# Optimization experiments

Measured on AMD Instinct MI355X. Metric: run time of the kernel, lower is better.

The kernel has to match this reference:

```python
import jax, jax.numpy as jnp
import numpy as np
import math

# Config (matches init_kwargs): ProphetNet-style ngram self-attention
T, B, E, H, NGRAM, NB, MAXD = 512, 4, 1024, 16, 2, 32, 128
HD = E // H
TGT = (1 + NGRAM) * T
NEG = -1e9


def _buckets(rel):
    # faithful numpy version of _relative_positions_bucket (bidirectional=False)
    n = np.maximum(-rel, 0)
    max_exact = NB // 2
    is_small = n < max_exact
    large = max_exact + np.log(np.maximum(n, 1) / max_exact) / math.log(MAXD / max_exact) * (NB - max_exact)
    large = np.minimum(large, NB - 1).astype(np.int32)
    return np.where(is_small, n.astype(np.int32), large)


def setup_inputs() -> dict:
    key = jax.random.key(0)
    ks = jax.random.split(key, 4)
    s = 0.02
    # position ids 1..T (ProphetNet positions start at 1); precompute bucket tables
    pos = np.arange(1, T + 1, dtype=np.int64)[None, :].repeat(B, axis=0)          # [B,T]
    main_rel = pos[:, None, :] - pos[:, :, None]                                  # [B,T,T]
    pred_keys = np.concatenate([pos - 1, pos], axis=-1)                           # [B,2T]
    pred_rel = pred_keys[:, None, :] - pos[:, :, None]                            # [B,T,2T]
    return {
        "query": jax.random.normal(ks[0], (TGT, B, E), jnp.float32),
        "in_proj_weight": jax.random.normal(ks[1], (3 * E, E), jnp.float32) * s,
        "in_proj_bias": jnp.zeros((3 * E,), jnp.float32),
        "rel_w": jax.random.normal(ks[2], (NB * H, E), jnp.float32) * s,
        "rel_b": jnp.zeros((NB * H,), jnp.float32),
        "out_w": jax.random.normal(ks[3], (E, E), jnp.float32) * s,
        "out_b": jnp.zeros((E,), jnp.float32),
        "main_buckets": jnp.asarray(_buckets(main_rel), jnp.int32),
        "predict_buckets": jnp.asarray(_buckets(pred_rel), jnp.int32),
    }


def reference(query, in_proj_weight, in_proj_bias, rel_w, rel_b, out_w, out_b,
              main_buckets, predict_buckets):
    scaling = HD ** -0.5
    qkv = query @ in_proj_weight.T + in_proj_bias                  # [TGT,B,3E]
    q, k, v = jnp.split(qkv, 3, axis=-1)
    q = q * scaling

    def heads(x):  # [TGT,B,E] -> [B*H, TGT, HD]
        return x.reshape(TGT, B * H, HD).transpose(1, 0, 2)

    q, k, v = heads(q), heads(k), heads(v)
    q_main, k_main, v_main = q[:, :T], k[:, :T], v[:, :T]

    def ngram_split(x):  # [B*H, NGRAM*T, HD] -> [N, B*H, T, HD]
        return x[:, T:].reshape(B * H, NGRAM, T, HD).transpose(1, 0, 2, 3)

    q_pred, k_pred, v_pred = ngram_split(q), ngram_split(k), ngram_split(v)
    h_main = query[:T]                                             # [T,B,E]
    h_pred = query[T:].reshape(NGRAM, T, B, E)

    # ---------- main stream ----------
    aw_main = jnp.einsum('bth,bsh->bts', q_main, k_main)           # [B*H,T,T]
    vals = h_main.transpose(1, 0, 2) @ rel_w.T + rel_b             # [B,T,NB*H]
    vals = vals.reshape(B, T, NB, H).transpose(0, 3, 1, 2)         # [B,H,T,NB]
    idx = jnp.broadcast_to(main_buckets[:, None], (B, H, T, T))
    rel_main = jnp.take_along_axis(vals, idx, axis=-1).reshape(B * H, T, T)
    causal = jnp.triu(jnp.full((T, T), NEG, jnp.float32), 1)       # self_attn_mask
    aw_main = jax.nn.softmax(aw_main + rel_main + causal[None], axis=-1)
    attn_main = jnp.einsum('bts,bsh->bth', aw_main, v_main)        # [B*H,T,HD]
    attn_main = attn_main.transpose(1, 0, 2).reshape(1, T, B, E)
    attn_main = attn_main @ out_w.T + out_b

    # ---------- ngram predict streams ----------
    k_ng = jnp.concatenate([jnp.broadcast_to(k_main[None], (NGRAM, B * H, T, HD)), k_pred], axis=2)
    v_ng = jnp.concatenate([jnp.broadcast_to(v_main[None], (NGRAM, B * H, T, HD)), v_pred], axis=2)
    aw_ng = jnp.einsum('nbtc,nbsc->nbts', q_pred, k_ng)            # [N,B*H,T,2T]
    valsn = h_pred.transpose(0, 2, 1, 3) @ rel_w.T + rel_b         # [N,B,T,NB*H]
    valsn = valsn.reshape(NGRAM, B, T, NB, H).transpose(0, 1, 4, 2, 3)  # [N,B,H,T,NB]
    idxn = jnp.broadcast_to(predict_buckets[None, :, None], (NGRAM, B, H, T, 2 * T))
    rel_ng = jnp.take_along_axis(valsn, idxn, axis=-1).reshape(NGRAM, B * H, T, 2 * T)
    # ngram_mask: main part causal, predict part only the matching position
    ng_mask = jnp.concatenate([causal, NEG * (1.0 - jnp.eye(T, dtype=jnp.float32))], axis=1)  # [T,2T]
    aw_ng = jax.nn.softmax(aw_ng + rel_ng + ng_mask[None, None], axis=-1)
    attn_ng = jnp.einsum('nbts,nbsc->nbtc', aw_ng, v_ng)           # [N,B*H,T,HD]
    attn_ng = attn_ng.transpose(0, 2, 1, 3).reshape(NGRAM, T, B, E)
    attn_ng = attn_ng @ out_w.T + out_b

    return jnp.concatenate([attn_main, attn_ng], axis=0).reshape(TGT, B, E)
```

## Files before the change

kernel.cpp:

```cpp
#include <hip/hip_runtime.h>
#include <hip/hip_bf16.h>
#include <math.h>

constexpr int T_ = 512;
constexpr int B_ = 4;
constexpr int E_ = 1024;
constexpr int H_ = 16;
constexpr int NGRAM_ = 2;
constexpr int TGT_ = (1 + NGRAM_) * T_;
constexpr int ROWS_ = TGT_ * B_;

typedef __bf16 bf16_t;
typedef __bf16 bf16x8 __attribute__((ext_vector_type(8)));
typedef __bf16 bf16x4 __attribute__((ext_vector_type(4)));
typedef float f32x4 __attribute__((ext_vector_type(4)));

#define GLL(gaddr, laddr)                                                     \
  __builtin_amdgcn_global_load_lds(                                           \
      (const __attribute__((address_space(1))) void*)(gaddr),                 \
      (__attribute__((address_space(3))) void*)(laddr), 16, 0, 0)

__global__ __launch_bounds__(256) void prep(
    const float* __restrict__ query, const float* __restrict__ ipw,
    const float* __restrict__ relw, const float* __restrict__ outw,
    bf16_t* __restrict__ qb, bf16_t* __restrict__ ipwb,
    bf16_t* __restrict__ relwb, bf16_t* __restrict__ outwb,
    const int* __restrict__ mbuck, const int* __restrict__ pbuck,
    unsigned char* __restrict__ lutM, unsigned char* __restrict__ lutP) {
  const int i = blockIdx.x * 256 + threadIdx.x;
  if (i < 512) {
    lutM[i] = (unsigned char)mbuck[(size_t)i * T_];
    lutP[i] = (unsigned char)pbuck[(size_t)i * (2 * T_)];
  }
  constexpr int N1 = ROWS_ * E_ / 4;
  constexpr int N2 = 3 * E_ * E_ / 4;
  constexpr int N3 = 512 * E_ / 4;
  constexpr int N4 = E_ * E_ / 4;
  const float4* src;
  bf16_t* dst;
  int j = i;
  if (i < N1) { src = (const float4*)query; dst = qb; }
  else if (i < N1 + N2) { src = (const float4*)ipw; dst = ipwb; j = i - N1; }
  else if (i < N1 + N2 + N3) { src = (const float4*)relw; dst = relwb; j = i - N1 - N2; }
  else if (i < N1 + N2 + N3 + N4) { src = (const float4*)outw; dst = outwb; j = i - N1 - N2 - N3; }
  else return;
  const float4 v = src[j];
  bf16x4 o;
  o[0] = (bf16_t)v.x; o[1] = (bf16_t)v.y;
  o[2] = (bf16_t)v.z; o[3] = (bf16_t)v.w;
  ((bf16x4*)dst)[j] = o;
}

__global__ __launch_bounds__(256) void transpose_v(
    const bf16_t* __restrict__ qkvb, bf16_t* __restrict__ vT) {
  __shared__ bf16_t tile[64][72];
  const int tb = blockIdx.x;
  const int bh = blockIdx.y;
  const int b = bh >> 4, h = bh & 15;
  const int tid = threadIdx.x;
  const int tau0 = tb * 64;
#pragma unroll
  for (int u = 0; u < 2; ++u) {
    const int c = u * 256 + tid;
    const int r = c >> 3, kc = c & 7;
    *(uint4*)&tile[r][kc * 8] = *(const uint4*)
        &qkvb[((size_t)(tau0 + r) * B_ + b) * 3072 + 2048 + h * 64 + kc * 8];
  }
  __syncthreads();
#pragma unroll
  for (int u = 0; u < 2; ++u) {
    const int c = u * 256 + tid;
    const int d = c >> 3, tc = c & 7;
    bf16x8 v;
#pragma unroll
    for (int i = 0; i < 8; ++i) v[i] = tile[tc * 8 + i][d];
    *(bf16x8*)&vT[((size_t)bh * 64 + d) * (size_t)TGT_ + tau0 + tc * 8] = v;
  }
}

__global__ __launch_bounds__(256, 4) void bgemm_proj(
    const bf16_t* __restrict__ A, const bf16_t* __restrict__ W,
    const float* __restrict__ ipb, const float* __restrict__ relb,
    bf16_t* __restrict__ qkvb, float* __restrict__ relv2) {
  __shared__ bf16_t As[128 * 64];
  __shared__ bf16_t Bs[128 * 64];

  const int tid = threadIdx.x;
  const int wave = tid >> 6, lane = tid & 63;
  const int wr = wave >> 1, wc = wave & 1;
  const int bm = blockIdx.y * 128, bn = blockIdx.x * 128;
  const int q = lane >> 4, ln = lane & 15;
  const int grow = tid >> 3;
  const int gcol = ((tid & 7) ^ (grow & 7)) * 8;

  f32x4 acc[4][4];
#pragma unroll
  for (int mi = 0; mi < 4; ++mi)
#pragma unroll
    for (int ni = 0; ni < 4; ++ni)
#pragma unroll
      for (int r = 0; r < 4; ++r) acc[mi][ni][r] = 0.f;

  const int co[2] = {((q) ^ (ln & 7)) * 8, ((4 + q) ^ (ln & 7)) * 8};

  for (int k0 = 0; k0 < 1024; k0 += 64) {
    __syncthreads();
#pragma unroll
    for (int p = 0; p < 4; ++p) {
      GLL(&A[(size_t)(bm + p * 32 + grow) * 1024 + k0 + gcol], &As[p * 2048 + tid * 8]);
      GLL(&W[(size_t)(bn + p * 32 + grow) * 1024 + k0 + gcol], &Bs[p * 2048 + tid * 8]);
    }
    __syncthreads();
#pragma unroll
    for (int t = 0; t < 2; ++t) {
      bf16x8 af[4], bf[4];
#pragma unroll
      for (int mi = 0; mi < 4; ++mi)
        af[mi] = *(const bf16x8*)&As[(wr * 64 + mi * 16 + ln) * 64 + co[t]];
#pragma unroll
      for (int ni = 0; ni < 4; ++ni)
        bf[ni] = *(const bf16x8*)&Bs[(wc * 64 + ni * 16 + ln) * 64 + co[t]];
#pragma unroll
      for (int mi = 0; mi < 4; ++mi)
#pragma unroll
        for (int ni = 0; ni < 4; ++ni)
          acc[mi][ni] = __builtin_amdgcn_mfma_f32_16x16x32_bf16(
              af[mi], bf[ni], acc[mi][ni], 0, 0, 0);
    }
  }

  if (bn < 3072) {
    const float sc = (bn < 1024) ? 0.125f : 1.0f;
#pragma unroll
    for (int mi = 0; mi < 4; ++mi) {
#pragma unroll
      for (int ni = 0; ni < 4; ++ni) {
        const int col = bn + wc * 64 + ni * 16 + ln;
        const float bv = ipb[col];
#pragma unroll
        for (int r = 0; r < 4; ++r) {
          const int row = bm + wr * 64 + mi * 16 + q * 4 + r;
          qkvb[(size_t)row * 3072 + col] = (bf16_t)((acc[mi][ni][r] + bv) * sc);
        }
      }
    }
  } else {
    const int cb = bn - 3072 + wc * 64;
    float4 rb4;
#pragma unroll
    for (int ni = 0; ni < 4; ++ni)
      ((float*)&rb4)[ni] = relb[cb + ni * 16 + ln];
    const int bkbase = cb >> 4;
#pragma unroll
    for (int mi = 0; mi < 4; ++mi) {
#pragma unroll
      for (int r = 0; r < 4; ++r) {
        const int row = bm + wr * 64 + mi * 16 + q * 4 + r;
        float4 v;
        v.x = acc[mi][0][r] + rb4.x;
        v.y = acc[mi][1][r] + rb4.y;
        v.z = acc[mi][2][r] + rb4.z;
        v.w = acc[mi][3][r] + rb4.w;
        *(float4*)&relv2[(size_t)row * 512 + ln * 32 + bkbase] = v;
      }
    }
  }
}

__global__ __launch_bounds__(256, 4) void bgemm_out(
    const bf16_t* __restrict__ A, const bf16_t* __restrict__ W,
    const float* __restrict__ bias, float* __restrict__ C, int N) {
  __shared__ bf16_t As[128 * 64];
  __shared__ bf16_t Bs[128 * 64];

  const int tid = threadIdx.x;
  const int wave = tid >> 6, lane = tid & 63;
  const int wr = wave >> 1, wc = wave & 1;
  const int bm = blockIdx.y * 128, bn = blockIdx.x * 128;
  const int q = lane >> 4, ln = lane & 15;
  const int grow = tid >> 3;
  const int gcol = ((tid & 7) ^ (grow & 7)) * 8;

  f32x4 acc[4][4];
#pragma unroll
  for (int mi = 0; mi < 4; ++mi)
#pragma unroll
    for (int ni = 0; ni < 4; ++ni)
#pragma unroll
      for (int r = 0; r < 4; ++r) acc[mi][ni][r] = 0.f;

  const int co[2] = {((q) ^ (ln & 7)) * 8, ((4 + q) ^ (ln & 7)) * 8};

  for (int k0 = 0; k0 < 1024; k0 += 64) {
    __syncthreads();
#pragma unroll
    for (int p = 0; p < 4; ++p) {
      GLL(&A[(size_t)(bm + p * 32 + grow) * 1024 + k0 + gcol], &As[p * 2048 + tid * 8]);
      GLL(&W[(size_t)(bn + p * 32 + grow) * 1024 + k0 + gcol], &Bs[p * 2048 + tid * 8]);
    }
    __syncthreads();
#pragma unroll
    for (int t = 0; t < 2; ++t) {
      bf16x8 af[4], bf[4];
#pragma unroll
      for (int mi = 0; mi < 4; ++mi)
        af[mi] = *(const bf16x8*)&As[(wr * 64 + mi * 16 + ln) * 64 + co[t]];
#pragma unroll
      for (int ni = 0; ni < 4; ++ni)
        bf[ni] = *(const bf16x8*)&Bs[(wc * 64 + ni * 16 + ln) * 64 + co[t]];
#pragma unroll
      for (int mi = 0; mi < 4; ++mi)
#pragma unroll
        for (int ni = 0; ni < 4; ++ni)
          acc[mi][ni] = __builtin_amdgcn_mfma_f32_16x16x32_bf16(
              af[mi], bf[ni], acc[mi][ni], 0, 0, 0);
    }
  }

#pragma unroll
  for (int mi = 0; mi < 4; ++mi) {
#pragma unroll
    for (int ni = 0; ni < 4; ++ni) {
      const int col = bn + wc * 64 + ni * 16 + ln;
      const float bv = bias[col];
#pragma unroll
      for (int r = 0; r < 4; ++r) {
        const int row = bm + wr * 64 + mi * 16 + q * 4 + r;
        C[(size_t)row * N + col] = acc[mi][ni][r] + bv;
      }
    }
  }
}

__global__ __launch_bounds__(256, 4) void flash_mfma(
    const bf16_t* __restrict__ qkvb, const bf16_t* __restrict__ vT,
    const float* __restrict__ relv2,
    const unsigned char* __restrict__ lutM, const unsigned char* __restrict__ lutP,
    bf16_t* __restrict__ attn) {
  __shared__ bf16_t Qs[64 * 64];
  __shared__ bf16_t Ks[64 * 64];
  __shared__ bf16_t Vts[64 * 64];
  __shared__ bf16_t Ps[4][16 * 64];
  __shared__ bf16_t biasS[64 * 33];
  __shared__ unsigned char lutS[512];

  const int qt = blockIdx.x, tq0 = qt * 64;
  const int bh = blockIdx.y, b = bh >> 4, h = bh & 15;
  const int z = blockIdx.z;
  const int tid = threadIdx.x;
  const int wave = tid >> 6, lane = tid & 63;
  const int q = lane >> 4, ln = lane & 15;
  const int m0 = wave * 16;
  const int qbase = (z == 0) ? tq0 : (T_ + (z - 1) * T_ + tq0);
  const int grow = tid >> 3;
  const int gcol = ((tid & 7) ^ (grow & 7)) * 8;

  if (tid < 128)
    ((int*)lutS)[tid] = ((const int*)(z == 0 ? lutM : lutP))[tid];

#pragma unroll
  for (int u = 0; u < 2; ++u) {
    const int sr = u * 32 + grow;
    GLL(&qkvb[((size_t)(qbase + sr) * B_ + b) * 3072 + h * 64 + gcol],
        &Qs[u * 2048 + tid * 8]);
  }
#pragma unroll
  for (int u = 0; u < 2; ++u) {
    const int c = u * 256 + tid;
    const int row = c >> 3, j4 = (c & 7) * 4;
    const float4 v = *(const float4*)
        &relv2[((size_t)(qbase + row) * B_ + b) * 512 + h * 32 + j4];
    biasS[row * 33 + j4 + 0] = (bf16_t)v.x;
    biasS[row * 33 + j4 + 1] = (bf16_t)v.y;
    biasS[row * 33 + j4 + 2] = (bf16_t)v.z;
    biasS[row * 33 + j4 + 3] = (bf16_t)v.w;
  }
  __syncthreads();

  const int co[2] = {((q) ^ (ln & 7)) * 8, ((4 + q) ^ (ln & 7)) * 8};

  bf16x8 aq[2];
  aq[0] = *(const bf16x8*)&Qs[(m0 + ln) * 64 + co[0]];
  aq[1] = *(const bf16x8*)&Qs[(m0 + ln) * 64 + co[1]];

  f32x4 Od[4];
  float lpart[4];
#pragma unroll
  for (int r = 0; r < 4; ++r) {
    lpart[r] = 0.f;
#pragma unroll
    for (int tc = 0; tc < 4; ++tc) Od[tc][r] = 0.f;
  }

  const int ntiles = qt + 1 + ((z > 0) ? 1 : 0);

  for (int j = 0; j < ntiles; ++j) {
    const bool extra = (z > 0) && (j > qt);
    const int krb = extra ? (T_ + (z - 1) * T_ + tq0) : j * 64;

    __syncthreads();
#pragma unroll
    for (int u = 0; u < 2; ++u) {
      const int sr = u * 32 + grow;
      GLL(&qkvb[((size_t)(krb + sr) * B_ + b) * 3072 + 1024 + h * 64 + gcol],
          &Ks[u * 2048 + tid * 8]);
      GLL(&vT[((size_t)bh * 64 + sr) * (size_t)TGT_ + krb + gcol],
          &Vts[u * 2048 + tid * 8]);
    }
    __syncthreads();

    f32x4 acc[4];
#pragma unroll
    for (int tc = 0; tc < 4; ++tc)
#pragma unroll
      for (int r = 0; r < 4; ++r) acc[tc][r] = 0.f;
#pragma unroll
    for (int tc = 0; tc < 4; ++tc) {
      const bf16x8 b0 = *(const bf16x8*)&Ks[(tc * 16 + ln) * 64 + co[0]];
      acc[tc] = __builtin_amdgcn_mfma_f32_16x16x32_bf16(aq[0], b0, acc[tc], 0, 0, 0);
      const bf16x8 b1 = *(const bf16x8*)&Ks[(tc * 16 + ln) * 64 + co[1]];
      acc[tc] = __builtin_amdgcn_mfma_f32_16x16x32_bf16(aq[1], b1, acc[tc], 0, 0, 0);
    }

#pragma unroll
    for (int r = 0; r < 4; ++r) {
      const int rloc = m0 + q * 4 + r;
      const int t = tq0 + rloc;
#pragma unroll
      for (int tc = 0; tc < 4; ++tc) {
        const int sl = tc * 16 + ln;
        bool valid;
        float bv;
        if (!extra) {
          valid = (j < qt) | (sl <= rloc);
          int d = t - (j * 64 + sl);
          d = d < 0 ? 0 : d;
          bv = (float)biasS[rloc * 33 + (int)lutS[d]];
        } else {
          valid = (sl == rloc);
          bv = (float)biasS[rloc * 33];
        }
        const float p = valid ? __expf(acc[tc][r] + bv) : 0.f;
        lpart[r] += p;
        const int pc = (tc * 2 + (ln >> 3)) ^ ((q * 4 + r) & 7);
        Ps[wave][(q * 4 + r) * 64 + pc * 8 + (ln & 7)] = (bf16_t)p;
      }
    }

    bf16x8 ap[2];
    ap[0] = *(const bf16x8*)&Ps[wave][ln * 64 + co[0]];
    ap[1] = *(const bf16x8*)&Ps[wave][ln * 64 + co[1]];
#pragma unroll
    for (int tc = 0; tc < 4; ++tc) {
      const bf16x8 v0 = *(const bf16x8*)&Vts[(tc * 16 + ln) * 64 + co[0]];
      Od[tc] = __builtin_amdgcn_mfma_f32_16x16x32_bf16(ap[0], v0, Od[tc], 0, 0, 0);
      const bf16x8 v1 = *(const bf16x8*)&Vts[(tc * 16 + ln) * 64 + co[1]];
      Od[tc] = __builtin_amdgcn_mfma_f32_16x16x32_bf16(ap[1], v1, Od[tc], 0, 0, 0);
    }
  }

#pragma unroll
  for (int r = 0; r < 4; ++r) {
    float l = lpart[r];
    l += __shfl_xor(l, 1, 16);
    l += __shfl_xor(l, 2, 16);
    l += __shfl_xor(l, 4, 16);
    l += __shfl_xor(l, 8, 16);
    const float inv = 1.f / l;
    const size_t rowbase =
        ((size_t)(qbase + m0 + q * 4 + r) * B_ + b) * (size_t)E_ + h * 64;
#pragma unroll
    for (int tc = 0; tc < 4; ++tc)
      attn[rowbase + tc * 16 + ln] = (bf16_t)(Od[tc][r] * inv);
  }
}

extern "C" void kernel_launch(void* const* d_in, const int* in_sizes, int n_in,
                              void* d_out, int out_size, void* d_ws, size_t ws_size,
                              hipStream_t stream) {
  const float* query = (const float*)d_in[0];
  const float* ipw   = (const float*)d_in[1];
  const float* ipb   = (const float*)d_in[2];
  const float* relw  = (const float*)d_in[3];
  const float* relb  = (const float*)d_in[4];
  const float* outw  = (const float*)d_in[5];
  const float* outb  = (const float*)d_in[6];
  const int*   mbuck = (const int*)d_in[7];
  const int*   pbuck = (const int*)d_in[8];
  float* out = (float*)d_out;

  bf16_t* qkvb  = (bf16_t*)d_ws;
  float*  relv2 = (float*)(qkvb + (size_t)ROWS_ * 3 * E_);
  bf16_t* qb    = (bf16_t*)(relv2 + (size_t)ROWS_ * 512);
  bf16_t* ipwb  = qb + (size_t)ROWS_ * E_;
  bf16_t* relwb = ipwb + (size_t)(3 * E_) * E_;
  bf16_t* outwb = relwb + (size_t)512 * E_;
  bf16_t* attnb = outwb + (size_t)E_ * E_;
  unsigned char* lutM = (unsigned char*)(attnb + (size_t)ROWS_ * E_);
  unsigned char* lutP = lutM + 512;
  bf16_t* vT = (bf16_t*)(lutP + 512);

  const dim3 blk(256);

  {
    const int ntot = (ROWS_ * E_ + 3 * E_ * E_ + 512 * E_ + E_ * E_) / 4;
    prep<<<dim3((ntot + 255) / 256), blk, 0, stream>>>(
        query, ipw, relw, outw, qb, ipwb, relwb, outwb, mbuck, pbuck, lutM, lutP);
  }

  bgemm_proj<<<dim3(3584 / 128, ROWS_ / 128), blk, 0, stream>>>(
      qb, ipwb, ipb, relb, qkvb, relv2);

  transpose_v<<<dim3(TGT_ / 64, B_ * H_), blk, 0, stream>>>(qkvb, vT);

  flash_mfma<<<dim3(T_ / 64, B_ * H_, 1 + NGRAM_), blk, 0, stream>>>(
      qkvb, vT, relv2, lutM, lutP, attnb);

  bgemm_out<<<dim3(E_ / 128, ROWS_ / 128), blk, 0, stream>>>(
      attnb, outwb, outb, out, E_);
}
```

Before: 251.6 us.

## Fuse main and ngram streams in one flash block to share K/V tiles

Each block now handles one query tile for all three streams (main plus two ngram) and loads each causal K/V tile once, reusing it across the three query sets. The extra self-position tiles are handled as trailing iterations, and block order is reversed so the longest causal blocks start first. This targets the repeated K/V global loads across the z dimension. In exchange the grid shrinks to a third, which lowers parallelism, and three accumulator sets raise register pressure.

```diff
diff --git a/kernel.cpp b/kernel.cpp
--- a/kernel.cpp
+++ b/kernel.cpp
@@ -237,66 +237,72 @@
     const float* __restrict__ relv2,
     const unsigned char* __restrict__ lutM, const unsigned char* __restrict__ lutP,
     bf16_t* __restrict__ attn) {
-  __shared__ bf16_t Qs[64 * 64];
   __shared__ bf16_t Ks[64 * 64];
   __shared__ bf16_t Vts[64 * 64];
   __shared__ bf16_t Ps[4][16 * 64];
-  __shared__ bf16_t biasS[64 * 33];
-  __shared__ unsigned char lutS[512];
-
-  const int qt = blockIdx.x, tq0 = qt * 64;
+  __shared__ bf16_t biasS[3][64 * 33];
+  __shared__ unsigned char lutMs[512];
+  __shared__ unsigned char lutPs[512];
+
+  const int qt = 7 - blockIdx.x, tq0 = qt * 64;
   const int bh = blockIdx.y, b = bh >> 4, h = bh & 15;
-  const int z = blockIdx.z;
   const int tid = threadIdx.x;
   const int wave = tid >> 6, lane = tid & 63;
   const int q = lane >> 4, ln = lane & 15;
   const int m0 = wave * 16;
-  const int qbase = (z == 0) ? tq0 : (T_ + (z - 1) * T_ + tq0);
   const int grow = tid >> 3;
   const int gcol = ((tid & 7) ^ (grow & 7)) * 8;
-
-  if (tid < 128)
-    ((int*)lutS)[tid] = ((const int*)(z == 0 ? lutM : lutP))[tid];
-
-#pragma unroll
-  for (int u = 0; u < 2; ++u) {
-    const int sr = u * 32 + grow;
-    GLL(&qkvb[((size_t)(qbase + sr) * B_ + b) * 3072 + h * 64 + gcol],
-        &Qs[u * 2048 + tid * 8]);
-  }
-#pragma unroll
-  for (int u = 0; u < 2; ++u) {
-    const int c = u * 256 + tid;
-    const int row = c >> 3, j4 = (c & 7) * 4;
-    const float4 v = *(const float4*)
-        &relv2[((size_t)(qbase + row) * B_ + b) * 512 + h * 32 + j4];
-    biasS[row * 33 + j4 + 0] = (bf16_t)v.x;
-    biasS[row * 33 + j4 + 1] = (bf16_t)v.y;
-    biasS[row * 33 + j4 + 2] = (bf16_t)v.z;
-    biasS[row * 33 + j4 + 3] = (bf16_t)v.w;
-  }
-  __syncthreads();
-
   const int co[2] = {((q) ^ (ln & 7)) * 8, ((4 + q) ^ (ln & 7)) * 8};
 
-  bf16x8 aq[2];
-  aq[0] = *(const bf16x8*)&Qs[(m0 + ln) * 64 + co[0]];
-  aq[1] = *(const bf16x8*)&Qs[(m0 + ln) * 64 + co[1]];
-
-  f32x4 Od[4];
-  float lpart[4];
-#pragma unroll
-  for (int r = 0; r < 4; ++r) {
-    lpart[r] = 0.f;
-#pragma unroll
-    for (int tc = 0; tc < 4; ++tc) Od[tc][r] = 0.f;
-  }
-
-  const int ntiles = qt + 1 + ((z > 0) ? 1 : 0);
+  if (tid < 128) ((int*)lutMs)[tid] = ((const int*)lutM)[tid];
+  else if (tid < 256) ((int*)lutPs)[tid - 128] = ((const int*)lutP)[tid - 128];
+
+#pragma unroll
+  for (int z = 0; z < 3; ++z) {
+#pragma unroll
+    for (int u = 0; u < 2; ++u) {
+      const int c = u * 256 + tid;
+      const int row = c >> 3, j4 = (c & 7) * 4;
+      const float4 v = *(const float4*)
+          &relv2[((size_t)(z * T_ + tq0 + row) * B_ + b) * 512 + h * 32 + j4];
+      biasS[z][row * 33 + j4 + 0] = (bf16_t)v.x;
+      biasS[z][row * 33 + j4 + 1] = (bf16_t)v.y;
+      biasS[z][row * 33 + j4 + 2] = (bf16_t)v.z;
+      biasS[z][row * 33 + j4 + 3] = (bf16_t)v.w;
+    }
+  }
+
+  bf16x8 aq[3][2];
+#pragma unroll
+  for (int z = 0; z < 3; ++z) {
+    __syncthreads();
+#pragma unroll
+    for (int u = 0; u < 2; ++u) {
+      const int sr = u * 32 + grow;
+      GLL(&qkvb[((size_t)(z * T_ + tq0 + sr) * B_ + b) * 3072 + h * 64 + gcol],
+          &Ks[u * 2048 + tid * 8]);
+    }
+    __syncthreads();
+    aq[z][0] = *(const bf16x8*)&Ks[(m0 + ln) * 64 + co[0]];
+    aq[z][1] = *(const bf16x8*)&Ks[(m0 + ln) * 64 + co[1]];
+  }
+
+  f32x4 Od[3][4];
+  float lpart[3][4];
+#pragma unroll
+  for (int z = 0; z < 3; ++z)
+#pragma unroll
+    for (int r = 0; r < 4; ++r) {
+      lpart[z][r] = 0.f;
+#pragma unroll
+      for (int tc = 0; tc < 4; ++tc) Od[z][tc][r] = 0.f;
+    }
+
+  const int ntiles = qt + 3;
 
   for (int j = 0; j < ntiles; ++j) {
-    const bool extra = (z > 0) && (j > qt);
-    const int krb = extra ? (T_ + (z - 1) * T_ + tq0) : j * 64;
+    const int ze = j - qt;
+    const int krb = (ze > 0) ? (ze * T_ + tq0) : j * 64;
 
     __syncthreads();
 #pragma unroll
@@ -309,69 +315,75 @@
     }
     __syncthreads();
 
-    f32x4 acc[4];
-#pragma unroll
-    for (int tc = 0; tc < 4; ++tc)
-#pragma unroll
-      for (int r = 0; r < 4; ++r) acc[tc][r] = 0.f;
-#pragma unroll
-    for (int tc = 0; tc < 4; ++tc) {
-      const bf16x8 b0 = *(const bf16x8*)&Ks[(tc * 16 + ln) * 64 + co[0]];
-      acc[tc] = __builtin_amdgcn_mfma_f32_16x16x32_bf16(aq[0], b0, acc[tc], 0, 0, 0);
-      const bf16x8 b1 = *(const bf16x8*)&Ks[(tc * 16 + ln) * 64 + co[1]];
-      acc[tc] = __builtin_amdgcn_mfma_f32_16x16x32_bf16(aq[1], b1, acc[tc], 0, 0, 0);
-    }
-
+    const int zlo = (ze > 0) ? ze : 0;
+    const int zhi = (ze > 0) ? ze : 2;
+    for (int z = zlo; z <= zhi; ++z) {
+      f32x4 acc[4];
+#pragma unroll
+      for (int tc = 0; tc < 4; ++tc)
+#pragma unroll
+        for (int r = 0; r < 4; ++r) acc[tc][r] = 0.f;
+#pragma unroll
+      for (int tc = 0; tc < 4; ++tc) {
+        const bf16x8 b0 = *(const bf16x8*)&Ks[(tc * 16 + ln) * 64 + co[0]];
+        acc[tc] = __builtin_amdgcn_mfma_f32_16x16x32_bf16(aq[z][0], b0, acc[tc], 0, 0, 0);
+        const bf16x8 b1 = *(const bf16x8*)&Ks[(tc * 16 + ln) * 64 + co[1]];
+        acc[tc] = __builtin_amdgcn_mfma_f32_16x16x32_bf16(aq[z][1], b1, acc[tc], 0, 0, 0);
+      }
+
+#pragma unroll
+      for (int r = 0; r < 4; ++r) {
+        const int rloc = m0 + q * 4 + r;
+#pragma unroll
+        for (int tc = 0; tc < 4; ++tc) {
+          const int sl = tc * 16 + ln;
+          bool valid;
+          float bv;
+          if (ze <= 0) {
+            valid = (j < qt) | (sl <= rloc);
+            int d = tq0 + rloc - (j * 64 + sl);
+            d = d < 0 ? 0 : d;
+            bv = (float)biasS[z][rloc * 33 + (int)(z == 0 ? lutMs[d] : lutPs[d])];
+          } else {
+            valid = (sl == rloc);
+            bv = (float)biasS[z][rloc * 33];
+          }
+          const float p = valid ? __expf(acc[tc][r] + bv) : 0.f;
+          lpart[z][r] += p;
+          const int pc = (tc * 2 + (ln >> 3)) ^ ((q * 4 + r) & 7);
+          Ps[wave][(q * 4 + r) * 64 + pc * 8 + (ln & 7)] = (bf16_t)p;
+        }
+      }
+
+      bf16x8 ap[2];
+      ap[0] = *(const bf16x8*)&Ps[wave][ln * 64 + co[0]];
+      ap[1] = *(const bf16x8*)&Ps[wave][ln * 64 + co[1]];
+#pragma unroll
+      for (int tc = 0; tc < 4; ++tc) {
+        const bf16x8 v0 = *(const bf16x8*)&Vts[(tc * 16 + ln) * 64 + co[0]];
+        Od[z][tc] = __builtin_amdgcn_mfma_f32_16x16x32_bf16(ap[0], v0, Od[z][tc], 0, 0, 0);
+        const bf16x8 v1 = *(const bf16x8*)&Vts[(tc * 16 + ln) * 64 + co[1]];
+        Od[z][tc] = __builtin_amdgcn_mfma_f32_16x16x32_bf16(ap[1], v1, Od[z][tc], 0, 0, 0);
+      }
+    }
+  }
+
+#pragma unroll
+  for (int z = 0; z < 3; ++z) {
 #pragma unroll
     for (int r = 0; r < 4; ++r) {
-      const int rloc = m0 + q * 4 + r;
-      const int t = tq0 + rloc;
-#pragma unroll
-      for (int tc = 0; tc < 4; ++tc) {
-        const int sl = tc * 16 + ln;
-        bool valid;
-        float bv;
-        if (!extra) {
-          valid = (j < qt) | (sl <= rloc);
-          int d = t - (j * 64 + sl);
-          d = d < 0 ? 0 : d;
-          bv = (float)biasS[rloc * 33 + (int)lutS[d]];
-        } else {
-          valid = (sl == rloc);
-          bv = (float)biasS[rloc * 33];
-        }
-        const float p = valid ? __expf(acc[tc][r] + bv) : 0.f;
-        lpart[r] += p;
-        const int pc = (tc * 2 + (ln >> 3)) ^ ((q * 4 + r) & 7);
-        Ps[wave][(q * 4 + r) * 64 + pc * 8 + (ln & 7)] = (bf16_t)p;
-      }
-    }
-
-    bf16x8 ap[2];
-    ap[0] = *(const bf16x8*)&Ps[wave][ln * 64 + co[0]];
-    ap[1] = *(const bf16x8*)&Ps[wave][ln * 64 + co[1]];
-#pragma unroll
-    for (int tc = 0; tc < 4; ++tc) {
-      const bf16x8 v0 = *(const bf16x8*)&Vts[(tc * 16 + ln) * 64 + co[0]];
-      Od[tc] = __builtin_amdgcn_mfma_f32_16x16x32_bf16(ap[0], v0, Od[tc], 0, 0, 0);
-      const bf16x8 v1 = *(const bf16x8*)&Vts[(tc * 16 + ln) * 64 + co[1]];
-      Od[tc] = __builtin_amdgcn_mfma_f32_16x16x32_bf16(ap[1], v1, Od[tc], 0, 0, 0);
-    }
-  }
-
-#pragma unroll
-  for (int r = 0; r < 4; ++r) {
-    float l = lpart[r];
-    l += __shfl_xor(l, 1, 16);
-    l += __shfl_xor(l, 2, 16);
-    l += __shfl_xor(l, 4, 16);
-    l += __shfl_xor(l, 8, 16);
-    const float inv = 1.f / l;
-    const size_t rowbase =
-        ((size_t)(qbase + m0 + q * 4 + r) * B_ + b) * (size_t)E_ + h * 64;
-#pragma unroll
-    for (int tc = 0; tc < 4; ++tc)
-      attn[rowbase + tc * 16 + ln] = (bf16_t)(Od[tc][r] * inv);
+      float l = lpart[z][r];
+      l += __shfl_xor(l, 1, 16);
+      l += __shfl_xor(l, 2, 16);
+      l += __shfl_xor(l, 4, 16);
+      l += __shfl_xor(l, 8, 16);
+      const float inv = 1.f / l;
+      const size_t rowbase =
+          ((size_t)(z * T_ + tq0 + m0 + q * 4 + r) * B_ + b) * (size_t)E_ + h * 64;
+#pragma unroll
+      for (int tc = 0; tc < 4; ++tc)
+        attn[rowbase + tc * 16 + ln] = (bf16_t)(Od[z][tc][r] * inv);
+    }
   }
 }
 
@@ -413,7 +425,7 @@
 
   transpose_v<<<dim3(TGT_ / 64, B_ * H_), blk, 0, stream>>>(qkvb, vT);
 
-  flash_mfma<<<dim3(T_ / 64, B_ * H_, 1 + NGRAM_), blk, 0, stream>>>(
+  flash_mfma<<<dim3(8, B_ * H_), blk, 0, stream>>>(
       qkvb, vT, relv2, lutM, lutP, attnb);
 
   bgemm_out<<<dim3(E_ / 128, ROWS_ / 128), blk, 0, stream>>>(
```

New measurement: 358.8 us. +42.6%, slower.
